# Kernel tuning notes

Hardware: AMD Instinct MI355X
Metric: run time of the kernel (lower is better)

Reference implementation:

```python
import jax, jax.numpy as jnp
import numpy as np

D_MODEL, D_K, D_V, H, B = 1024, 64, 64, 16, 32768


def _xavier(key, fan_in, fan_out):
    std = float(np.sqrt(2.0 / (fan_in + fan_out)))
    return jax.random.normal(key, (fan_in, fan_out), dtype=jnp.float32) * std


def setup_inputs() -> dict:
    key = jax.random.key(0)
    ks = jax.random.split(key, 7)
    return {
        "queries": jax.random.normal(ks[0], (B, D_MODEL), dtype=jnp.float32),
        "keys": jax.random.normal(ks[1], (B, D_MODEL), dtype=jnp.float32),
        "values": jax.random.normal(ks[2], (B, D_MODEL), dtype=jnp.float32),
        "Wq": _xavier(ks[3], D_MODEL, H * D_K),
        "bq": jnp.zeros((H * D_K,), jnp.float32),
        "Wk": _xavier(ks[4], D_MODEL, H * D_K),
        "bk": jnp.zeros((H * D_K,), jnp.float32),
        "Wv": _xavier(ks[5], D_MODEL, H * D_V),
        "bv": jnp.zeros((H * D_V,), jnp.float32),
        "Wo": _xavier(ks[6], H * D_V, D_MODEL),
        "bo": jnp.zeros((D_MODEL,), jnp.float32),
    }


def reference(queries, keys, values, Wq, bq, Wk, bk, Wv, bv, Wo, bo):
    b = queries.shape[0]
    q = (queries @ Wq + bq).reshape(b, H, D_K)   # (b, h, d_k)
    k = (keys @ Wk + bk).reshape(b, H, D_K)      # (b, h, d_k)
    v = (values @ Wv + bv).reshape(b, H, D_V)    # (b, h, d_v)
    # attention over heads: (b, h, h)
    att = jnp.einsum('bhd,bgd->bhg', q, k) / jnp.sqrt(jnp.float32(D_K))
    att = jax.nn.softmax(att, axis=-1)
    out = jnp.einsum('bhg,bgd->bhd', att, v).reshape(b, H * D_V)
    return out @ Wo + bo
```

## Files before the change

kernel.cpp:

```cpp
#include <hip/hip_runtime.h>

typedef __attribute__((ext_vector_type(8))) unsigned short u16x8;
typedef __attribute__((ext_vector_type(8))) short s16x8;
typedef __attribute__((ext_vector_type(4))) float f32x4;

#define D_MODEL 1024
#define NROWS 32768
#define BK 64
#define NT 16

__device__ __forceinline__ unsigned short f2bf(float f) {
  union { float f; unsigned int u; } c; c.f = f;
  return (unsigned short)((c.u + 0x7fffu + ((c.u >> 16) & 1u)) >> 16);
}
__device__ __forceinline__ float bf2f(unsigned short h) {
  union { unsigned int u; float f; } c; c.u = ((unsigned int)h) << 16;
  return c.f;
}

__device__ __forceinline__ void gload_lds16(const void* gsrc, void* ldst) {
  const __attribute__((address_space(1))) void* g =
      reinterpret_cast<const __attribute__((address_space(1))) void*>(
          reinterpret_cast<unsigned long long>(gsrc));
  __attribute__((address_space(3))) void* l =
      reinterpret_cast<__attribute__((address_space(3))) void*>(
          static_cast<unsigned int>(reinterpret_cast<unsigned long long>(ldst)));
  __builtin_amdgcn_global_load_lds(g, l, 16, 0, 0);
}

#define BAR() asm volatile("s_barrier" ::: "memory")

__global__ __launch_bounds__(256) void wtrans_kernel(
    const float* __restrict__ W0, const float* __restrict__ W1,
    const float* __restrict__ W2, const float* __restrict__ W3,
    unsigned short* __restrict__ T0, unsigned short* __restrict__ T1,
    unsigned short* __restrict__ T2, unsigned short* __restrict__ T3) {
  const float* W = blockIdx.z == 0 ? W0 : blockIdx.z == 1 ? W1 : blockIdx.z == 2 ? W2 : W3;
  unsigned short* T = blockIdx.z == 0 ? T0 : blockIdx.z == 1 ? T1 : blockIdx.z == 2 ? T2 : T3;
  __shared__ float tile[32][33];
  const int tx = threadIdx.x & 31, ty = threadIdx.x >> 5;
  const int n0 = blockIdx.x * 32, k0 = blockIdx.y * 32;
#pragma unroll
  for (int i = 0; i < 4; ++i)
    tile[ty + 8 * i][tx] = W[(size_t)(k0 + ty + 8 * i) * D_MODEL + n0 + tx];
  __syncthreads();
#pragma unroll
  for (int i = 0; i < 4; ++i)
    T[(size_t)(n0 + ty + 8 * i) * D_MODEL + k0 + tx] = f2bf(tile[tx][ty + 8 * i]);
}

__global__ __launch_bounds__(256) void xconvert(
    const float* __restrict__ X0, const float* __restrict__ X1, const float* __restrict__ X2,
    unsigned short* __restrict__ Y0, unsigned short* __restrict__ Y1,
    unsigned short* __restrict__ Y2) {
  const float* X = blockIdx.z == 0 ? X0 : blockIdx.z == 1 ? X1 : X2;
  unsigned short* Y = blockIdx.z == 0 ? Y0 : blockIdx.z == 1 ? Y1 : Y2;
  const int NCH = (NROWS * D_MODEL) / 8;
  for (int c = blockIdx.x * 256 + threadIdx.x; c < NCH; c += gridDim.x * 256) {
    f32x4 f0 = *(const f32x4*)(X + (size_t)c * 8);
    f32x4 f1 = *(const f32x4*)(X + (size_t)c * 8 + 4);
    u16x8 h;
#pragma unroll
    for (int e = 0; e < 4; ++e) { h[e] = f2bf(f0[e]); h[4 + e] = f2bf(f1[e]); }
    *(u16x8*)(Y + (size_t)c * 8) = h;
  }
}

#define MFMA16(p, A00, A01, A10, A11)                                                        \
  _Pragma("unroll") for (int n = 0; n < 4; ++n) {                                            \
    acc[2*(p)][n]   = __builtin_amdgcn_mfma_f32_16x16x32_bf16(A00, bfr[n][0], acc[2*(p)][n], 0, 0, 0);   \
    acc[2*(p)][n]   = __builtin_amdgcn_mfma_f32_16x16x32_bf16(A01, bfr[n][1], acc[2*(p)][n], 0, 0, 0);   \
    acc[2*(p)+1][n] = __builtin_amdgcn_mfma_f32_16x16x32_bf16(A10, bfr[n][0], acc[2*(p)+1][n], 0, 0, 0); \
    acc[2*(p)+1][n] = __builtin_amdgcn_mfma_f32_16x16x32_bf16(A11, bfr[n][1], acc[2*(p)+1][n], 0, 0, 0); \
  }

#define LDA_(Ac, m, ksoff) (*(const s16x8*)((Ac) + (wm * 128 + (m) * 16 + lrow) * 128 + (ksoff)))
#define LDB_(Bc, n, ksoff) (*(const s16x8*)((Bc) + (wn * 64 + (n) * 16 + lrow) * 128 + (ksoff)))

template <bool OUT_BF16>
__device__ __forceinline__ void gemm8p_body(
    const unsigned short* __restrict__ A, const unsigned short* __restrict__ BT,
    const float* __restrict__ bias, void* __restrict__ Cp, char* smem) {
  const int tid = threadIdx.x;
  const int lane = tid & 63, wid = tid >> 6;
  const int wm = wid >> 2, wn = wid & 3;
  const int lrow = lane & 15, lkg = lane >> 4;

  const int id = blockIdx.y * gridDim.x + blockIdx.x;
  const int sw = (id & 7) * 64 + (id >> 3);
  const int mbase = (sw >> 2) * 256;
  const int nbase = (sw & 3) * 256;

  const int sgoff = (((tid & 7) ^ ((tid >> 3) & 7)) * 8);
  const int srow = tid >> 3;
  const int soff0 = ((0 + lkg) ^ (lrow & 7)) * 16;
  const int soff1 = ((4 + lkg) ^ (lrow & 7)) * 16;
  const int ldsw = wid * 1024;

  auto stA = [&](char* dst, int u, int half) {
    const unsigned short* G =
        A + (size_t)(mbase + half * 128 + srow) * D_MODEL + u * BK + sgoff;
    char* L = dst + half * 16384 + ldsw;
    gload_lds16(G, L);
    gload_lds16(G + (size_t)64 * D_MODEL, L + 8192);
  };
  auto stB = [&](char* dst, int u, int half) {
    const unsigned short* G =
        BT + (size_t)(nbase + half * 128 + srow) * D_MODEL + u * BK + sgoff;
    char* L = dst + half * 16384 + ldsw;
    gload_lds16(G, L);
    gload_lds16(G + (size_t)64 * D_MODEL, L + 8192);
  };

  f32x4 acc[8][4];
  f32x4 zero = {0.f, 0.f, 0.f, 0.f};
#pragma unroll
  for (int m = 0; m < 8; ++m)
#pragma unroll
    for (int n = 0; n < 4; ++n) acc[m][n] = zero;
  s16x8 bfr[4][2];

  char* Acur = smem;
  char* Anxt = smem + 32768;
  char* Apf  = smem + 65536;
  char* Bcur = smem + 98304;
  char* Bnxt = smem + 131072;

  stA(Acur, 0, 0); stA(Acur, 0, 1); stB(Bcur, 0, 0); stB(Bcur, 0, 1);
  stA(Anxt, 1, 0); stA(Anxt, 1, 1); stB(Bnxt, 1, 0); stB(Bnxt, 1, 1);
  asm volatile("s_waitcnt vmcnt(8)" ::: "memory");
  BAR();

#pragma unroll 1
  for (int u = 0; u < NT; ++u) {
    const bool pf = (u + 2 < NT);
    {
      s16x8 a00 = LDA_(Acur, 0, soff0), a01 = LDA_(Acur, 0, soff1);
      s16x8 a10 = LDA_(Acur, 1, soff0), a11 = LDA_(Acur, 1, soff1);
#pragma unroll
      for (int n = 0; n < 4; ++n) { bfr[n][0] = LDB_(Bcur, n, soff0); bfr[n][1] = LDB_(Bcur, n, soff1); }
      if (pf) stA(Apf, u + 2, 0);
      BAR();
      __builtin_amdgcn_s_setprio(1);
      MFMA16(0, a00, a01, a10, a11);
      __builtin_amdgcn_s_setprio(0);
      BAR();
    }
    {
      s16x8 a00 = LDA_(Acur, 2, soff0), a01 = LDA_(Acur, 2, soff1);
      s16x8 a10 = LDA_(Acur, 3, soff0), a11 = LDA_(Acur, 3, soff1);
      if (pf) stA(Apf, u + 2, 1);
      BAR();
      __builtin_amdgcn_s_setprio(1);
      MFMA16(1, a00, a01, a10, a11);
      __builtin_amdgcn_s_setprio(0);
      BAR();
    }
    {
      s16x8 a00 = LDA_(Acur, 4, soff0), a01 = LDA_(Acur, 4, soff1);
      s16x8 a10 = LDA_(Acur, 5, soff0), a11 = LDA_(Acur, 5, soff1);
      if (pf) stB(Bcur, u + 2, 0);
      BAR();
      __builtin_amdgcn_s_setprio(1);
      MFMA16(2, a00, a01, a10, a11);
      __builtin_amdgcn_s_setprio(0);
      BAR();
    }
    {
      s16x8 a00 = LDA_(Acur, 6, soff0), a01 = LDA_(Acur, 6, soff1);
      s16x8 a10 = LDA_(Acur, 7, soff0), a11 = LDA_(Acur, 7, soff1);
      if (pf) {
        stB(Bcur, u + 2, 1);
        asm volatile("s_waitcnt vmcnt(8)" ::: "memory");
      } else {
        asm volatile("s_waitcnt vmcnt(0)" ::: "memory");
      }
      BAR();
      __builtin_amdgcn_s_setprio(1);
      MFMA16(3, a00, a01, a10, a11);
      __builtin_amdgcn_s_setprio(0);
      BAR();
    }
    char* t = Acur; Acur = Anxt; Anxt = Apf; Apf = t;
    char* tb = Bcur; Bcur = Bnxt; Bnxt = tb;
  }

  const size_t crow0 = mbase + wm * 128;
  const int ccol0 = nbase + wn * 64;
#pragma unroll
  for (int m = 0; m < 8; ++m) {
#pragma unroll
    for (int n = 0; n < 4; ++n) {
      const int col = ccol0 + n * 16 + lrow;
      const float bv = bias[col];
#pragma unroll
      for (int r = 0; r < 4; ++r) {
        const size_t row = crow0 + m * 16 + lkg * 4 + r;
        const float v = acc[m][n][r] + bv;
        if constexpr (OUT_BF16)
          ((unsigned short*)Cp)[row * D_MODEL + col] = f2bf(v);
        else
          ((float*)Cp)[row * D_MODEL + col] = v;
      }
    }
  }
}

__global__ __launch_bounds__(512, 1) void qkv_gemm8(
    const unsigned short* __restrict__ Xq, const unsigned short* __restrict__ Xk,
    const unsigned short* __restrict__ Xv,
    const unsigned short* __restrict__ WqT, const unsigned short* __restrict__ WkT,
    const unsigned short* __restrict__ WvT,
    const float* __restrict__ bq, const float* __restrict__ bk, const float* __restrict__ bv,
    unsigned short* __restrict__ Qb, unsigned short* __restrict__ Kb,
    unsigned short* __restrict__ Vb) {
  extern __shared__ char smem[];
  const int z = blockIdx.z;
  gemm8p_body<true>(z == 0 ? Xq : z == 1 ? Xk : Xv,
                    z == 0 ? WqT : z == 1 ? WkT : WvT,
                    z == 0 ? bq : z == 1 ? bk : bv,
                    z == 0 ? (void*)Qb : z == 1 ? (void*)Kb : (void*)Vb, smem);
}

__global__ __launch_bounds__(512, 1) void out_gemm8(
    const unsigned short* __restrict__ Ob, const unsigned short* __restrict__ WoT,
    const float* __restrict__ bo, float* __restrict__ out) {
  extern __shared__ char smem[];
  gemm8p_body<false>(Ob, WoT, bo, out, smem);
}

__global__ __launch_bounds__(256) void attn_kernel(
    const unsigned short* __restrict__ Qb, const unsigned short* __restrict__ Kb,
    const unsigned short* __restrict__ Vb, unsigned short* __restrict__ Ob) {
  __shared__ __align__(16) unsigned short sm[4][3][16 * 72];
  const int tid = threadIdx.x, lane = tid & 63, wid = tid >> 6;
  const size_t row = (size_t)blockIdx.x * 4 + wid;
  const unsigned short* srcs[3] = {Qb + row * 1024, Kb + row * 1024, Vb + row * 1024};
#pragma unroll
  for (int m = 0; m < 3; ++m) {
#pragma unroll
    for (int i = 0; i < 2; ++i) {
      int c = lane * 2 + i;
      int h = c >> 3, col = (c & 7) * 8;
      *(u16x8*)&sm[wid][m][h * 72 + col] = *(const u16x8*)(srcs[m] + h * 64 + col);
    }
  }
  __syncthreads();

  const int h = lane & 15, gq = lane >> 4;
  float s[4] = {0.f, 0.f, 0.f, 0.f};
#pragma unroll
  for (int dc = 0; dc < 8; ++dc) {
    u16x8 qv = *(const u16x8*)&sm[wid][0][h * 72 + dc * 8];
    float qf[8];
#pragma unroll
    for (int e = 0; e < 8; ++e) qf[e] = bf2f(qv[e]);
#pragma unroll
    for (int j = 0; j < 4; ++j) {
      u16x8 kv = *(const u16x8*)&sm[wid][1][(gq * 4 + j) * 72 + dc * 8];
#pragma unroll
      for (int e = 0; e < 8; ++e) s[j] += qf[e] * bf2f(kv[e]);
    }
  }
  float mx = s[0];
#pragma unroll
  for (int j = 0; j < 4; ++j) { s[j] *= 0.125f; mx = fmaxf(mx * (j == 0 ? 0.125f : 1.f), s[j]); }
  mx = fmaxf(mx, __shfl_xor(mx, 16, 64));
  mx = fmaxf(mx, __shfl_xor(mx, 32, 64));
  float p[4], sum = 0.f;
#pragma unroll
  for (int j = 0; j < 4; ++j) { p[j] = __expf(s[j] - mx); sum += p[j]; }
  sum += __shfl_xor(sum, 16, 64);
  sum += __shfl_xor(sum, 32, 64);
  const float rinv = 1.0f / sum;
  float pall[16];
#pragma unroll
  for (int t = 0; t < 4; ++t)
#pragma unroll
    for (int j = 0; j < 4; ++j) pall[t * 4 + j] = __shfl(p[j], h + 16 * t, 64);
  float o[16];
#pragma unroll
  for (int e = 0; e < 16; ++e) o[e] = 0.f;
  const int db = gq * 16;
#pragma unroll
  for (int g = 0; g < 16; ++g) {
    float pg = pall[g];
    u16x8 v0 = *(const u16x8*)&sm[wid][2][g * 72 + db];
    u16x8 v1 = *(const u16x8*)&sm[wid][2][g * 72 + db + 8];
#pragma unroll
    for (int e = 0; e < 8; ++e) { o[e] += pg * bf2f(v0[e]); o[8 + e] += pg * bf2f(v1[e]); }
  }
  u16x8 r0, r1;
#pragma unroll
  for (int e = 0; e < 8; ++e) { r0[e] = f2bf(o[e] * rinv); r1[e] = f2bf(o[8 + e] * rinv); }
  unsigned short* dst = Ob + row * 1024 + h * 64 + db;
  *(u16x8*)dst = r0;
  *(u16x8*)(dst + 8) = r1;
}

extern "C" void kernel_launch(void* const* d_in, const int* in_sizes, int n_in,
                              void* d_out, int out_size, void* d_ws, size_t ws_size,
                              hipStream_t stream) {
  const float* queries = (const float*)d_in[0];
  const float* keys    = (const float*)d_in[1];
  const float* values  = (const float*)d_in[2];
  const float* Wq = (const float*)d_in[3];
  const float* bq = (const float*)d_in[4];
  const float* Wk = (const float*)d_in[5];
  const float* bk = (const float*)d_in[6];
  const float* Wv = (const float*)d_in[7];
  const float* bv = (const float*)d_in[8];
  const float* Wo = (const float*)d_in[9];
  const float* bo = (const float*)d_in[10];
  float* out = (float*)d_out;

  unsigned short* ws = (unsigned short*)d_ws;
  const size_t WE = (size_t)1024 * 1024;
  const size_t XE = (size_t)NROWS * 1024;
  unsigned short* WqT = ws;
  unsigned short* WkT = WqT + WE;
  unsigned short* WvT = WkT + WE;
  unsigned short* WoT = WvT + WE;
  unsigned short* Xcq = WoT + WE;
  unsigned short* Xck = Xcq + XE;
  unsigned short* Xcv = Xck + XE;
  unsigned short* Qb  = Xcv + XE;
  unsigned short* Kb  = Qb + XE;
  unsigned short* Vb  = Kb + XE;
  unsigned short* Ob  = Xcq;

  hipFuncSetAttribute((const void*)qkv_gemm8, hipFuncAttributeMaxDynamicSharedMemorySize, 163840);
  hipFuncSetAttribute((const void*)out_gemm8, hipFuncAttributeMaxDynamicSharedMemorySize, 163840);

  wtrans_kernel<<<dim3(32, 32, 4), 256, 0, stream>>>(Wq, Wk, Wv, Wo, WqT, WkT, WvT, WoT);
  xconvert<<<dim3(2048, 1, 3), 256, 0, stream>>>(queries, keys, values, Xcq, Xck, Xcv);
  qkv_gemm8<<<dim3(4, 128, 3), 512, 163840, stream>>>(
      Xcq, Xck, Xcv, WqT, WkT, WvT, bq, bk, bv, Qb, Kb, Vb);
  attn_kernel<<<dim3(NROWS / 4), 256, 0, stream>>>(Qb, Kb, Vb, Ob);
  out_gemm8<<<dim3(4, 128, 1), 512, 163840, stream>>>(Ob, WoT, bo, out);
}
```

Measured before the change: 486.5 us.

## Fuse fp32-to-bf16 input conversion into QKV GEMM via producer warps

Removes the separate xconvert pass and instead adds 4 producer waves to the QKV GEMM block that load fp32 activations, convert them with v_cvt_pk_bf16_f32, and write swizzled bf16 A tiles into LDS. The 8 consumer waves keep using the triple-buffered A and double-buffered B pipeline, with barriers paired to stay in lockstep with the producers. This drops the round trip of bf16 copies of X through global memory. In exchange the GEMM block grows to 768 threads with heavy register use in the producers, and correctness depends on the barrier counts matching exactly between the two roles. Ob gets its own workspace region instead of reusing the X buffer.

```diff
diff --git a/kernel.cpp b/kernel.cpp
--- a/kernel.cpp
+++ b/kernel.cpp
@@ -3,6 +3,7 @@
 typedef __attribute__((ext_vector_type(8))) unsigned short u16x8;
 typedef __attribute__((ext_vector_type(8))) short s16x8;
 typedef __attribute__((ext_vector_type(4))) float f32x4;
+typedef __attribute__((ext_vector_type(2))) unsigned int u32x2;
 
 #define D_MODEL 1024
 #define NROWS 32768
@@ -16,6 +17,11 @@
 __device__ __forceinline__ float bf2f(unsigned short h) {
   union { unsigned int u; float f; } c; c.u = ((unsigned int)h) << 16;
   return c.f;
+}
+__device__ __forceinline__ unsigned int cvtpk_bf16(float lo, float hi) {
+  unsigned int r;
+  asm("v_cvt_pk_bf16_f32 %0, %1, %2" : "=v"(r) : "v"(lo), "v"(hi));
+  return r;
 }
 
 __device__ __forceinline__ void gload_lds16(const void* gsrc, void* ldst) {
@@ -49,23 +55,6 @@
     T[(size_t)(n0 + ty + 8 * i) * D_MODEL + k0 + tx] = f2bf(tile[tx][ty + 8 * i]);
 }
 
-__global__ __launch_bounds__(256) void xconvert(
-    const float* __restrict__ X0, const float* __restrict__ X1, const float* __restrict__ X2,
-    unsigned short* __restrict__ Y0, unsigned short* __restrict__ Y1,
-    unsigned short* __restrict__ Y2) {
-  const float* X = blockIdx.z == 0 ? X0 : blockIdx.z == 1 ? X1 : X2;
-  unsigned short* Y = blockIdx.z == 0 ? Y0 : blockIdx.z == 1 ? Y1 : Y2;
-  const int NCH = (NROWS * D_MODEL) / 8;
-  for (int c = blockIdx.x * 256 + threadIdx.x; c < NCH; c += gridDim.x * 256) {
-    f32x4 f0 = *(const f32x4*)(X + (size_t)c * 8);
-    f32x4 f1 = *(const f32x4*)(X + (size_t)c * 8 + 4);
-    u16x8 h;
-#pragma unroll
-    for (int e = 0; e < 4; ++e) { h[e] = f2bf(f0[e]); h[4 + e] = f2bf(f1[e]); }
-    *(u16x8*)(Y + (size_t)c * 8) = h;
-  }
-}
-
 #define MFMA16(p, A00, A01, A10, A11)                                                        \
   _Pragma("unroll") for (int n = 0; n < 4; ++n) {                                            \
     acc[2*(p)][n]   = __builtin_amdgcn_mfma_f32_16x16x32_bf16(A00, bfr[n][0], acc[2*(p)][n], 0, 0, 0);   \
@@ -77,10 +66,192 @@
 #define LDA_(Ac, m, ksoff) (*(const s16x8*)((Ac) + (wm * 128 + (m) * 16 + lrow) * 128 + (ksoff)))
 #define LDB_(Bc, n, ksoff) (*(const s16x8*)((Bc) + (wn * 64 + (n) * 16 + lrow) * 128 + (ksoff)))
 
-template <bool OUT_BF16>
-__device__ __forceinline__ void gemm8p_body(
+
+#define PLOAD(S, u, k0)                                                                   \
+  _Pragma("unroll") for (int k = (k0); k < (k0) + 8; ++k)                                 \
+    S[k] = *(const f32x4*)(Abase + (size_t)(16 * k) * D_MODEL + (size_t)(u) * BK);
+
+#define PWRITE(S, dst, k0)                                                                \
+  _Pragma("unroll") for (int k = (k0); k < (k0) + 8; ++k) {                               \
+    const int r = pr + 16 * k;                                                            \
+    u32x2 wv;                                                                             \
+    wv[0] = cvtpk_bf16(S[k][0], S[k][1]);                                                 \
+    wv[1] = cvtpk_bf16(S[k][2], S[k][3]);                                                 \
+    *(u32x2*)((dst) + (r >> 7) * 16384 + (r & 127) * 128 +                                \
+              (((pc >> 1) ^ (r & 7)) * 16) + (pc & 1) * 8) = wv;                          \
+  }
+
+#define PROD_TILE(u, SL, SW)                                                              \
+  {                                                                                       \
+    const bool ld = ((u) + 2 < NT);                                                       \
+    const bool wr = ((u) + 1 < NT);                                                       \
+    if (ld) { PLOAD(SL, (u) + 2, 0) }                                                     \
+    BAR(); BAR();                                                                         \
+    if (ld) { PLOAD(SL, (u) + 2, 8) }                                                     \
+    BAR(); BAR();                                                                         \
+    if (wr) { PWRITE(SW, Pnxt, 0) }                                                       \
+    BAR(); BAR();                                                                         \
+    if (wr) { PWRITE(SW, Pnxt, 8) }                                                       \
+    BAR();                                                                                \
+    asm volatile("s_waitcnt lgkmcnt(0)" ::: "memory");                                    \
+    BAR();                                                                                \
+    char* t_ = Pcur; Pcur = Pnxt; Pnxt = Ppf; Ppf = t_;                                   \
+  }
+
+__global__ __launch_bounds__(768, 3) void qkv_gemm8p(
+    const float* __restrict__ Xq, const float* __restrict__ Xk, const float* __restrict__ Xv,
+    const unsigned short* __restrict__ WqT, const unsigned short* __restrict__ WkT,
+    const unsigned short* __restrict__ WvT,
+    const float* __restrict__ bq, const float* __restrict__ bk, const float* __restrict__ bv,
+    unsigned short* __restrict__ Qb, unsigned short* __restrict__ Kb,
+    unsigned short* __restrict__ Vb) {
+  extern __shared__ char smem[];
+  const int z = blockIdx.z;
+  const float* A32 = z == 0 ? Xq : z == 1 ? Xk : Xv;
+  const unsigned short* BT = z == 0 ? WqT : z == 1 ? WkT : WvT;
+  const float* bias = z == 0 ? bq : z == 1 ? bk : bv;
+  unsigned short* C = z == 0 ? Qb : z == 1 ? Kb : Vb;
+
+  const int tid = threadIdx.x;
+  const int id = blockIdx.y * gridDim.x + blockIdx.x;
+  const int sw = (id & 7) * 64 + (id >> 3);
+  const int mbase = (sw >> 2) * 256;
+  const int nbase = (sw & 3) * 256;
+
+  if (tid < 512) {
+    const int lane = tid & 63, wid = tid >> 6;
+    const int wm = wid >> 2, wn = wid & 3;
+    const int lrow = lane & 15, lkg = lane >> 4;
+    const int sgoff = (((tid & 7) ^ ((tid >> 3) & 7)) * 8);
+    const int srow = tid >> 3;
+    const int soff0 = ((0 + lkg) ^ (lrow & 7)) * 16;
+    const int soff1 = ((4 + lkg) ^ (lrow & 7)) * 16;
+    const int ldsw = wid * 1024;
+
+    auto stB = [&](char* dst, int u, int half) {
+      const unsigned short* G =
+          BT + (size_t)(nbase + half * 128 + srow) * D_MODEL + u * BK + sgoff;
+      char* L = dst + half * 16384 + ldsw;
+      gload_lds16(G, L);
+      gload_lds16(G + (size_t)64 * D_MODEL, L + 8192);
+    };
+
+    f32x4 acc[8][4];
+    f32x4 zero = {0.f, 0.f, 0.f, 0.f};
+#pragma unroll
+    for (int m = 0; m < 8; ++m)
+#pragma unroll
+      for (int n = 0; n < 4; ++n) acc[m][n] = zero;
+    s16x8 bfr[4][2];
+
+    char* Acur = smem;
+    char* Anxt = smem + 32768;
+    char* Apf  = smem + 65536;
+    char* Bcur = smem + 98304;
+    char* Bnxt = smem + 131072;
+
+    stB(Bcur, 0, 0); stB(Bcur, 0, 1);
+    stB(Bnxt, 1, 0); stB(Bnxt, 1, 1);
+    asm volatile("s_waitcnt vmcnt(4)" ::: "memory");
+    BAR();
+
+#pragma unroll 1
+    for (int u = 0; u < NT; ++u) {
+      const bool pf = (u + 2 < NT);
+      {
+        s16x8 a00 = LDA_(Acur, 0, soff0), a01 = LDA_(Acur, 0, soff1);
+        s16x8 a10 = LDA_(Acur, 1, soff0), a11 = LDA_(Acur, 1, soff1);
+#pragma unroll
+        for (int n = 0; n < 4; ++n) { bfr[n][0] = LDB_(Bcur, n, soff0); bfr[n][1] = LDB_(Bcur, n, soff1); }
+        BAR();
+        __builtin_amdgcn_s_setprio(1);
+        MFMA16(0, a00, a01, a10, a11);
+        __builtin_amdgcn_s_setprio(0);
+        BAR();
+      }
+      {
+        s16x8 a00 = LDA_(Acur, 2, soff0), a01 = LDA_(Acur, 2, soff1);
+        s16x8 a10 = LDA_(Acur, 3, soff0), a11 = LDA_(Acur, 3, soff1);
+        BAR();
+        __builtin_amdgcn_s_setprio(1);
+        MFMA16(1, a00, a01, a10, a11);
+        __builtin_amdgcn_s_setprio(0);
+        BAR();
+      }
+      {
+        s16x8 a00 = LDA_(Acur, 4, soff0), a01 = LDA_(Acur, 4, soff1);
+        s16x8 a10 = LDA_(Acur, 5, soff0), a11 = LDA_(Acur, 5, soff1);
+        if (pf) stB(Bcur, u + 2, 0);
+        BAR();
+        __builtin_amdgcn_s_setprio(1);
+        MFMA16(2, a00, a01, a10, a11);
+        __builtin_amdgcn_s_setprio(0);
+        BAR();
+      }
+      {
+        s16x8 a00 = LDA_(Acur, 6, soff0), a01 = LDA_(Acur, 6, soff1);
+        s16x8 a10 = LDA_(Acur, 7, soff0), a11 = LDA_(Acur, 7, soff1);
+        if (pf) {
+          stB(Bcur, u + 2, 1);
+          asm volatile("s_waitcnt vmcnt(4)" ::: "memory");
+        } else {
+          asm volatile("s_waitcnt vmcnt(0)" ::: "memory");
+        }
+        BAR();
+        __builtin_amdgcn_s_setprio(1);
+        MFMA16(3, a00, a01, a10, a11);
+        __builtin_amdgcn_s_setprio(0);
+        BAR();
+      }
+      char* t = Acur; Acur = Anxt; Anxt = Apf; Apf = t;
+      char* tb = Bcur; Bcur = Bnxt; Bnxt = tb;
+    }
+
+    const size_t crow0 = mbase + wm * 128;
+    const int ccol0 = nbase + wn * 64;
+#pragma unroll
+    for (int m = 0; m < 8; ++m) {
+#pragma unroll
+      for (int n = 0; n < 4; ++n) {
+        const int col = ccol0 + n * 16 + lrow;
+        const float bv = bias[col];
+#pragma unroll
+        for (int r = 0; r < 4; ++r) {
+          const size_t row = crow0 + m * 16 + lkg * 4 + r;
+          C[row * D_MODEL + col] = f2bf(acc[m][n][r] + bv);
+        }
+      }
+    }
+  } else {
+    const int pt = tid - 512;
+    const int pr = pt >> 4;
+    const int pc = pt & 15;
+    const float* Abase = A32 + (size_t)(mbase + pr) * D_MODEL + pc * 4;
+
+    char* Pcur = smem;
+    char* Pnxt = smem + 32768;
+    char* Ppf  = smem + 65536;
+
+    f32x4 S0[16], S1[16];
+
+    PLOAD(S0, 0, 0) PLOAD(S0, 0, 8)
+    PWRITE(S0, Pcur, 0) PWRITE(S0, Pcur, 8)
+    PLOAD(S1, 1, 0) PLOAD(S1, 1, 8)
+    asm volatile("s_waitcnt lgkmcnt(0)" ::: "memory");
+    BAR();
+
+#pragma unroll 1
+    for (int uu = 0; uu < NT; uu += 2) {
+      PROD_TILE(uu, S0, S1)
+      PROD_TILE(uu + 1, S1, S0)
+    }
+  }
+}
+
+__global__ __launch_bounds__(512, 1) void out_gemm8(
     const unsigned short* __restrict__ A, const unsigned short* __restrict__ BT,
-    const float* __restrict__ bias, void* __restrict__ Cp, char* smem) {
+    const float* __restrict__ bias, float* __restrict__ Cp) {
+  extern __shared__ char smem[];
   const int tid = threadIdx.x;
   const int lane = tid & 63, wid = tid >> 6;
   const int wm = wid >> 2, wn = wid & 3;
@@ -196,37 +367,10 @@
 #pragma unroll
       for (int r = 0; r < 4; ++r) {
         const size_t row = crow0 + m * 16 + lkg * 4 + r;
-        const float v = acc[m][n][r] + bv;
-        if constexpr (OUT_BF16)
-          ((unsigned short*)Cp)[row * D_MODEL + col] = f2bf(v);
-        else
-          ((float*)Cp)[row * D_MODEL + col] = v;
-      }
-    }
-  }
-}
-
-__global__ __launch_bounds__(512, 1) void qkv_gemm8(
-    const unsigned short* __restrict__ Xq, const unsigned short* __restrict__ Xk,
-    const unsigned short* __restrict__ Xv,
-    const unsigned short* __restrict__ WqT, const unsigned short* __restrict__ WkT,
-    const unsigned short* __restrict__ WvT,
-    const float* __restrict__ bq, const float* __restrict__ bk, const float* __restrict__ bv,
-    unsigned short* __restrict__ Qb, unsigned short* __restrict__ Kb,
-    unsigned short* __restrict__ Vb) {
-  extern __shared__ char smem[];
-  const int z = blockIdx.z;
-  gemm8p_body<true>(z == 0 ? Xq : z == 1 ? Xk : Xv,
-                    z == 0 ? WqT : z == 1 ? WkT : WvT,
-                    z == 0 ? bq : z == 1 ? bk : bv,
-                    z == 0 ? (void*)Qb : z == 1 ? (void*)Kb : (void*)Vb, smem);
-}
-
-__global__ __launch_bounds__(512, 1) void out_gemm8(
-    const unsigned short* __restrict__ Ob, const unsigned short* __restrict__ WoT,
-    const float* __restrict__ bo, float* __restrict__ out) {
-  extern __shared__ char smem[];
-  gemm8p_body<false>(Ob, WoT, bo, out, smem);
+        Cp[row * D_MODEL + col] = acc[m][n][r] + bv;
+      }
+    }
+  }
 }
 
 __global__ __launch_bounds__(256) void attn_kernel(
@@ -321,21 +465,17 @@
   unsigned short* WkT = WqT + WE;
   unsigned short* WvT = WkT + WE;
   unsigned short* WoT = WvT + WE;
-  unsigned short* Xcq = WoT + WE;
-  unsigned short* Xck = Xcq + XE;
-  unsigned short* Xcv = Xck + XE;
-  unsigned short* Qb  = Xcv + XE;
+  unsigned short* Qb  = WoT + WE;
   unsigned short* Kb  = Qb + XE;
   unsigned short* Vb  = Kb + XE;
-  unsigned short* Ob  = Xcq;
-
-  hipFuncSetAttribute((const void*)qkv_gemm8, hipFuncAttributeMaxDynamicSharedMemorySize, 163840);
+  unsigned short* Ob  = Vb + XE;
+
+  hipFuncSetAttribute((const void*)qkv_gemm8p, hipFuncAttributeMaxDynamicSharedMemorySize, 163840);
   hipFuncSetAttribute((const void*)out_gemm8, hipFuncAttributeMaxDynamicSharedMemorySize, 163840);
 
   wtrans_kernel<<<dim3(32, 32, 4), 256, 0, stream>>>(Wq, Wk, Wv, Wo, WqT, WkT, WvT, WoT);
-  xconvert<<<dim3(2048, 1, 3), 256, 0, stream>>>(queries, keys, values, Xcq, Xck, Xcv);
-  qkv_gemm8<<<dim3(4, 128, 3), 512, 163840, stream>>>(
-      Xcq, Xck, Xcv, WqT, WkT, WvT, bq, bk, bv, Qb, Kb, Vb);
+  qkv_gemm8p<<<dim3(4, 128, 3), 768, 163840, stream>>>(
+      queries, keys, values, WqT, WkT, WvT, bq, bk, bv, Qb, Kb, Vb);
   attn_kernel<<<dim3(NROWS / 4), 256, 0, stream>>>(Qb, Kb, Vb, Ob);
   out_gemm8<<<dim3(4, 128, 1), 512, 163840, stream>>>(Ob, WoT, bo, out);
 }
```

Result: slower. 819.9 us (+68.5%).
